# Optimization experiments

Hardware: AMD Instinct MI355X
Metric: run time of the kernel (lower is better)

## Reference

```python
import jax, jax.numpy as jnp
import numpy as np

TIME_SCALE = 10.0
EPS = 1e-5


def _ln(x, g, b):
    m = jnp.mean(x, axis=-1, keepdims=True)
    v = jnp.mean((x - m) ** 2, axis=-1, keepdims=True)
    return (x - m) * jax.lax.rsqrt(v + EPS) * g + b


def setup_inputs() -> dict:
    key = jax.random.key(0)
    ks = jax.random.split(key, 16)
    B, S, D, H, C = 128, 2048, 67, 256, 1

    def lin(k, fan_in, shape):
        return (jax.random.uniform(k, shape, jnp.float32) * 2.0 - 1.0) / np.sqrt(fan_in)

    inp = {
        "x": jax.random.normal(ks[0], (B, S, D), jnp.float32),
        "dt": jax.random.uniform(ks[1], (B, S, 1), jnp.float32),
        # input LayerNorm
        "ln_in_g": jnp.ones((D,), jnp.float32),
        "ln_in_b": jnp.zeros((D,), jnp.float32),
        # feature projection: Linear(D,H) + LayerNorm(H) (+SiLU)
        "proj_W": lin(ks[2], D, (D, H)),
        "proj_b": jnp.zeros((H,), jnp.float32),
        "ln_p_g": jnp.ones((H,), jnp.float32),
        "ln_p_b": jnp.zeros((H,), jnp.float32),
        # CfC cell: four linears from concat([x_t, h]) (2H -> H)
        "W_ff1": lin(ks[3], 2 * H, (2 * H, H)),
        "b_ff1": jnp.zeros((H,), jnp.float32),
        "W_ff2": lin(ks[4], 2 * H, (2 * H, H)),
        "b_ff2": jnp.zeros((H,), jnp.float32),
        "W_ta": lin(ks[5], 2 * H, (2 * H, H)),
        "b_ta": jnp.zeros((H,), jnp.float32),
        "W_tb": lin(ks[6], 2 * H, (2 * H, H)),
        "b_tb": jnp.zeros((H,), jnp.float32),
        # event head: LayerNorm(H) + Linear(H, C)
        "head_g": jnp.ones((H,), jnp.float32),
        "head_b": jnp.zeros((H,), jnp.float32),
        "head_W": lin(ks[7], H, (H, C)),
        "head_bias": jnp.zeros((C,), jnp.float32),
    }
    return inp


def reference(x, dt, ln_in_g, ln_in_b, proj_W, proj_b, ln_p_g, ln_p_b,
              W_ff1, b_ff1, W_ff2, b_ff2, W_ta, b_ta, W_tb, b_tb,
              head_g, head_b, head_W, head_bias):
    B = x.shape[0]
    H = W_ff1.shape[1]

    xn = _ln(x, ln_in_g, ln_in_b)                      # [B,S,D]
    feat = jax.nn.silu(_ln(xn @ proj_W + proj_b, ln_p_g, ln_p_b))  # [B,S,H]

    xs = jnp.swapaxes(feat, 0, 1)                      # [S,B,H] time-major
    dts = jnp.swapaxes(dt * TIME_SCALE, 0, 1)          # [S,B,1]

    def step(h, inp):
        xt, dtt = inp
        z = jnp.concatenate([xt, h], axis=-1)          # [B,2H]
        ff1 = jnp.tanh(z @ W_ff1 + b_ff1)
        ff2 = jnp.tanh(z @ W_ff2 + b_ff2)
        t_interp = jax.nn.sigmoid((z @ W_ta + b_ta) * dtt + (z @ W_tb + b_tb))
        h_new = ff1 * (1.0 - t_interp) + t_interp * ff2
        return h_new, h_new

    h0 = jnp.zeros((B, H), x.dtype)
    _, hs = jax.lax.scan(step, h0, (xs, dts))          # hs: [S,B,H]
    seq = jnp.swapaxes(hs, 0, 1)                       # [B,S,H]
    logits = _ln(seq, head_g, head_b) @ head_W + head_bias  # [B,S,C]
    return logits
```

## Files before the change

kernel.cpp:

```cpp
#include <hip/hip_runtime.h>


typedef __bf16 bf16x8 __attribute__((ext_vector_type(8)));
typedef float f32x4 __attribute__((ext_vector_type(4)));
typedef int i32x4 __attribute__((ext_vector_type(4)));

#define DEVFN static __device__ __forceinline__

DEVFN float bf2f(unsigned short u){ return __uint_as_float(((unsigned)u) << 16); }
DEVFN unsigned short f2bf(float f){
  unsigned x = __float_as_uint(f);
  return (unsigned short)((x + 0x7FFFu + ((x >> 16) & 1u)) >> 16);
}
DEVFN float sigm(float x){ return 1.f / (1.f + __expf(-x)); }
DEVFN float tanh_f(float x){ return 1.f - 2.f / (__expf(2.f * x) + 1.f); }

#define GLD_LDS16(g, l) \
  __builtin_amdgcn_global_load_lds((const __attribute__((address_space(1))) void*)(g), \
                                   (__attribute__((address_space(3))) void*)(l), 16, 0, 0)

static constexpr int BB = 128;
static constexpr int SS = 2048;
static constexpr int DD = 67;

static constexpr size_t OFF_WXT   = 0;
static constexpr size_t OFF_WQ    = 524288;
static constexpr size_t OFF_SW    = 786432;
static constexpr size_t OFF_BIAS4 = 790528;
static constexpr size_t OFF_PWT   = 794624;
static constexpr size_t OFF_GW    = 843776;
static constexpr size_t OFF_SCAL  = 844800;
static constexpr size_t OFF_HST   = 845824;
static constexpr size_t OFF_FEAT  = 878592;

__global__ __launch_bounds__(256) void prep_kernel(
    const float* __restrict__ proj_W,
    const float* __restrict__ W_ff1, const float* __restrict__ b_ff1,
    const float* __restrict__ W_ff2, const float* __restrict__ b_ff2,
    const float* __restrict__ W_ta,  const float* __restrict__ b_ta,
    const float* __restrict__ W_tb,  const float* __restrict__ b_tb,
    const float* __restrict__ head_g, const float* __restrict__ head_b,
    const float* __restrict__ head_W, const float* __restrict__ head_bias,
    unsigned short* __restrict__ WxT, signed char* __restrict__ wq,
    float* __restrict__ sw, float* __restrict__ bias4,
    unsigned short* __restrict__ PWT, float* __restrict__ gW, float* __restrict__ scal)
{
  __shared__ float red[8];
  int bid = blockIdx.x, t = threadIdx.x;
  int wv = t >> 6, ln = t & 63;
  if (bid < 1024) {
    int J = bid, col = J & 255, which = J >> 8;
    const float* Wsrc = which == 0 ? W_ff1 : which == 1 ? W_ff2 : which == 2 ? W_ta : W_tb;
    const float* bsrc = which == 0 ? b_ff1 : which == 1 ? b_ff2 : which == 2 ? b_ta : b_tb;
    float w = Wsrc[t * 256 + col];
    WxT[J * 256 + t] = f2bf(w);
    if (t == 0) bias4[J] = bsrc[col];
  } else if (bid < 2048) {
    int J = bid - 1024, col = J & 255, which = J >> 8;
    const float* Wsrc = which == 0 ? W_ff1 : which == 1 ? W_ff2 : which == 2 ? W_ta : W_tb;
    float w = Wsrc[(256 + t) * 256 + col];
    float a = fabsf(w);
    for (int m = 32; m >= 1; m >>= 1) a = fmaxf(a, __shfl_xor(a, m, 64));
    if (ln == 0) red[wv] = a;
    __syncthreads();
    a = fmaxf(fmaxf(red[0], red[1]), fmaxf(red[2], red[3]));
    float scale = (a > 0.f) ? a * (1.f / 127.f) : 1.f;
    int q = (int)rintf(w / scale);
    q = q > 127 ? 127 : (q < -127 ? -127 : q);
    {
      int g = which, j = col, k = t;
      int wavw = (g << 1) | (j >> 7);
      int lane = ((k & 63) >> 4) * 16 + (j & 15);
      int tt = (j & 127) >> 4;
      int kt = k >> 6;
      size_t dst = (size_t)(wavw * 64 + lane) * 512 + (size_t)(tt * 4 + kt) * 16 + (size_t)(k & 15);
      wq[dst] = (signed char)q;
    }
    if (t == 0) sw[J] = scale;
  } else {
    for (int idx = t; idx < 256 * 96; idx += 256) {
      int j = idx / 96, d = idx % 96;
      float v = (d < DD) ? proj_W[d * 256 + j] : 0.f;
      PWT[idx] = f2bf(v);
    }
    float gw = head_g[t] * head_W[t];
    gW[t] = gw;
    float bw = head_b[t] * head_W[t];
    float s1 = gw, s2 = bw;
    for (int m = 32; m >= 1; m >>= 1) { s1 += __shfl_xor(s1, m, 64); s2 += __shfl_xor(s2, m, 64); }
    if (ln == 0) { red[wv] = s1; red[4 + wv] = s2; }
    __syncthreads();
    if (t == 0) {
      scal[0] = red[0] + red[1] + red[2] + red[3];
      scal[1] = red[4] + red[5] + red[6] + red[7] + head_bias[0];
    }
  }
}

__global__ __launch_bounds__(512) void feat_kernel(
    const float* __restrict__ x, const float* __restrict__ ln_in_g, const float* __restrict__ ln_in_b,
    const float* __restrict__ proj_b, const float* __restrict__ ln_p_g, const float* __restrict__ ln_p_b,
    const unsigned short* __restrict__ PWT, unsigned short* __restrict__ feat,
    int s0, int C, int cshift)
{
  __shared__ __align__(16) unsigned short XA[64 * 104];
  __shared__ __align__(16) unsigned short XB[256 * 96];
  __shared__ float partS[64][4], partQ[64][4], statM[64], statI[64];
  int tid = threadIdx.x, w = tid >> 6, lane = tid & 63;
  int r0 = blockIdx.x * 64;

  {
    float g1v = (lane < 67) ? ln_in_g[lane] : 0.f;
    float b1v = (lane < 67) ? ln_in_b[lane] : 0.f;
    float g2v = (lane < 3) ? ln_in_g[64 + lane] : 0.f;
    float b2v = (lane < 3) ? ln_in_b[64 + lane] : 0.f;
    for (int i = 0; i < 8; ++i) {
      int rl = w * 8 + i;
      int r = r0 + rl;
      int bb = r >> cshift, cs = r & (C - 1);
      const float* xr = x + (size_t)(bb * SS + s0 + cs) * DD;
      float v0 = (lane < 67) ? xr[lane] : 0.f;
      float v1 = (lane < 3) ? xr[64 + lane] : 0.f;
      float s = v0 + v1, q = v0 * v0 + v1 * v1;
      for (int m = 32; m >= 1; m >>= 1) { s += __shfl_xor(s, m, 64); q += __shfl_xor(q, m, 64); }
      float mean = s * (1.f / 67.f);
      float var = q * (1.f / 67.f) - mean * mean;
      float inv = rsqrtf(var + 1e-5f);
      float xn0 = (v0 - mean) * inv * g1v + b1v;
      float xn1 = (v1 - mean) * inv * g2v + b2v;
      XA[rl * 104 + lane] = (lane < 67) ? f2bf(xn0) : (unsigned short)0;
      if (lane < 40) XA[rl * 104 + 64 + lane] = (lane < 3) ? f2bf(xn1) : (unsigned short)0;
    }
  }
  {
    const unsigned int* src = (const unsigned int*)PWT;
    unsigned int* dst = (unsigned int*)XB;
    for (int idx = tid; idx < 256 * 48; idx += 512) dst[idx] = src[idx];
  }
  __syncthreads();

  int wm = w >> 2, wn = w & 3;
  f32x4 acc[2][4];
  #pragma unroll
  for (int mt = 0; mt < 2; ++mt)
    #pragma unroll
    for (int nt = 0; nt < 4; ++nt) acc[mt][nt] = (f32x4){0.f, 0.f, 0.f, 0.f};
  #pragma unroll
  for (int ks = 0; ks < 3; ++ks) {
    int k = ks * 32 + (lane >> 4) * 8;
    bf16x8 a[2], b[4];
    #pragma unroll
    for (int mt = 0; mt < 2; ++mt) {
      int row = wm * 32 + mt * 16 + (lane & 15);
      a[mt] = *reinterpret_cast<const bf16x8*>(&XA[row * 104 + k]);
    }
    #pragma unroll
    for (int nt = 0; nt < 4; ++nt) {
      int col = wn * 64 + nt * 16 + (lane & 15);
      b[nt] = *reinterpret_cast<const bf16x8*>(&XB[col * 96 + k]);
    }
    #pragma unroll
    for (int mt = 0; mt < 2; ++mt)
      #pragma unroll
      for (int nt = 0; nt < 4; ++nt)
        acc[mt][nt] = __builtin_amdgcn_mfma_f32_16x16x32_bf16(a[mt], b[nt], acc[mt][nt], 0, 0, 0);
  }
  #pragma unroll
  for (int nt = 0; nt < 4; ++nt) {
    int col = wn * 64 + nt * 16 + (lane & 15);
    float pb = proj_b[col];
    #pragma unroll
    for (int mt = 0; mt < 2; ++mt)
      #pragma unroll
      for (int r = 0; r < 4; ++r) acc[mt][nt][r] += pb;
  }
  #pragma unroll
  for (int mt = 0; mt < 2; ++mt) {
    #pragma unroll
    for (int r = 0; r < 4; ++r) {
      float s = 0.f, q = 0.f;
      #pragma unroll
      for (int nt = 0; nt < 4; ++nt) { float v = acc[mt][nt][r]; s += v; q += v * v; }
      for (int m = 1; m < 16; m <<= 1) { s += __shfl_xor(s, m, 16); q += __shfl_xor(q, m, 16); }
      if ((lane & 15) == 0) {
        int row = wm * 32 + mt * 16 + (lane >> 4) * 4 + r;
        partS[row][wn] = s; partQ[row][wn] = q;
      }
    }
  }
  __syncthreads();
  if (tid < 64) {
    float s = partS[tid][0] + partS[tid][1] + partS[tid][2] + partS[tid][3];
    float q = partQ[tid][0] + partQ[tid][1] + partQ[tid][2] + partQ[tid][3];
    float mean = s * (1.f / 256.f);
    float var = q * (1.f / 256.f) - mean * mean;
    statM[tid] = mean; statI[tid] = rsqrtf(var + 1e-5f);
  }
  __syncthreads();
  #pragma unroll
  for (int nt = 0; nt < 4; ++nt) {
    int col = wn * 64 + nt * 16 + (lane & 15);
    float gc = ln_p_g[col], bc = ln_p_b[col];
    #pragma unroll
    for (int mt = 0; mt < 2; ++mt)
      #pragma unroll
      for (int r = 0; r < 4; ++r) {
        int row = wm * 32 + mt * 16 + (lane >> 4) * 4 + r;
        float v = acc[mt][nt][r];
        float y = (v - statM[row]) * statI[row] * gc + bc;
        float sl = y * sigm(y);
        feat[(size_t)(r0 + row) * 256 + col] = f2bf(sl);
      }
  }
}

__global__ __launch_bounds__(256, 2) void gemm_kernel(
    const unsigned short* __restrict__ feat, const unsigned short* __restrict__ WxT,
    const float* __restrict__ bias4, unsigned short* __restrict__ pre)
{
  __shared__ __align__(16) unsigned short Abuf[128 * 64];
  __shared__ __align__(16) unsigned short Bbuf[128 * 64];
  int tid = threadIdx.x, w = tid >> 6, lane = tid & 63;
  int m0 = blockIdx.x * 128, n0 = blockIdx.y * 128;
  int wm = w >> 1, wn = w & 1;
  f32x4 acc[4][4];
  #pragma unroll
  for (int i = 0; i < 4; ++i)
    #pragma unroll
    for (int j = 0; j < 4; ++j) acc[i][j] = (f32x4){0.f, 0.f, 0.f, 0.f};

  #pragma unroll 1
  for (int ks = 0; ks < 4; ++ks) {
    int k0 = ks * 64;
    #pragma unroll
    for (int i = 0; i < 4; ++i) {
      int c = i * 256 + tid;
      int row = c >> 3, cc = c & 7;
      const unsigned short* ga = feat + (size_t)(m0 + row) * 256 + (k0 + cc * 8);
      const unsigned short* gb = WxT + (size_t)(n0 + row) * 256 + (k0 + cc * 8);
      char* la = (char*)Abuf + (size_t)(i * 256 + w * 64) * 16;
      char* lb = (char*)Bbuf + (size_t)(i * 256 + w * 64) * 16;
      GLD_LDS16(ga, la);
      GLD_LDS16(gb, lb);
    }
    __syncthreads();
    #pragma unroll
    for (int kk = 0; kk < 2; ++kk) {
      int k = kk * 32 + (lane >> 4) * 8;
      bf16x8 a[4], b[4];
      #pragma unroll
      for (int mt = 0; mt < 4; ++mt) {
        int row = wm * 64 + mt * 16 + (lane & 15);
        a[mt] = *reinterpret_cast<const bf16x8*>(&Abuf[row * 64 + k]);
      }
      #pragma unroll
      for (int nt = 0; nt < 4; ++nt) {
        int col = wn * 64 + nt * 16 + (lane & 15);
        b[nt] = *reinterpret_cast<const bf16x8*>(&Bbuf[col * 64 + k]);
      }
      #pragma unroll
      for (int mt = 0; mt < 4; ++mt)
        #pragma unroll
        for (int nt = 0; nt < 4; ++nt)
          acc[mt][nt] = __builtin_amdgcn_mfma_f32_16x16x32_bf16(a[mt], b[nt], acc[mt][nt], 0, 0, 0);
    }
    __syncthreads();
  }
  #pragma unroll
  for (int nt = 0; nt < 4; ++nt) {
    int col = n0 + wn * 64 + nt * 16 + (lane & 15);
    float bv = bias4[col];
    #pragma unroll
    for (int mt = 0; mt < 4; ++mt)
      #pragma unroll
      for (int r = 0; r < 4; ++r) {
        int row = m0 + wm * 64 + mt * 16 + (lane >> 4) * 4 + r;
        pre[(size_t)row * 1024 + col] = f2bf(acc[mt][nt][r] + bv);
      }
  }
}

#define WRA(n, val) asm volatile("v_accvgpr_write_b32 a" #n ", %0" :: "v"(val) : "a" #n)
#define WR4(n0,n1,n2,n3, q) \
  do { WRA(n0,(q).x); WRA(n1,(q).y); WRA(n2,(q).z); WRA(n3,(q).w); } while (0)
#define MFMA_AB(acc, af, b0, b1) \
  asm volatile("v_mfma_i32_16x16x64_i8 %0, %1, a[" #b0 ":" #b1 "], %2" \
               : "=&v"(acc) : "v"(af), "v"(acc))

__global__ __attribute__((amdgpu_flat_work_group_size(512, 512)))
           __attribute__((amdgpu_waves_per_eu(2, 2)))
void scan_kernel(
    const unsigned short* __restrict__ pre, const float* __restrict__ dt,
    const signed char* __restrict__ wq, const float* __restrict__ sw,
    int* __restrict__ hstate, unsigned short* __restrict__ hseq, int s0, int C)
{
  __shared__ int hq2[2][64];
  __shared__ int gsh[1024];
  int tid = threadIdx.x, w = tid >> 6, l = tid & 63;
  int b = blockIdx.x;

  {
    const int4* wp = (const int4*)(wq + (size_t)tid * 512);
    int4 q0, q1, q2, q3, q4, q5, q6, q7;
    q0=wp[0]; q1=wp[1]; q2=wp[2]; q3=wp[3]; q4=wp[4]; q5=wp[5]; q6=wp[6]; q7=wp[7];
    WR4(0,1,2,3,q0);     WR4(4,5,6,7,q1);     WR4(8,9,10,11,q2);    WR4(12,13,14,15,q3);
    WR4(16,17,18,19,q4); WR4(20,21,22,23,q5); WR4(24,25,26,27,q6);  WR4(28,29,30,31,q7);
    q0=wp[8]; q1=wp[9]; q2=wp[10]; q3=wp[11]; q4=wp[12]; q5=wp[13]; q6=wp[14]; q7=wp[15];
    WR4(32,33,34,35,q0); WR4(36,37,38,39,q1); WR4(40,41,42,43,q2);  WR4(44,45,46,47,q3);
    WR4(48,49,50,51,q4); WR4(52,53,54,55,q5); WR4(56,57,58,59,q6);  WR4(60,61,62,63,q7);
    q0=wp[16]; q1=wp[17]; q2=wp[18]; q3=wp[19]; q4=wp[20]; q5=wp[21]; q6=wp[22]; q7=wp[23];
    WR4(64,65,66,67,q0); WR4(68,69,70,71,q1); WR4(72,73,74,75,q2);  WR4(76,77,78,79,q3);
    WR4(80,81,82,83,q4); WR4(84,85,86,87,q5); WR4(88,89,90,91,q6);  WR4(92,93,94,95,q7);
    q0=wp[24]; q1=wp[25]; q2=wp[26]; q3=wp[27]; q4=wp[28]; q5=wp[29]; q6=wp[30]; q7=wp[31];
    WR4(96,97,98,99,q0);   WR4(100,101,102,103,q1); WR4(104,105,106,107,q2); WR4(108,109,110,111,q3);
    WR4(112,113,114,115,q4); WR4(116,117,118,119,q5); WR4(120,121,122,123,q6); WR4(124,125,126,127,q7);
  }

  float sc0 = 0.f, sc1 = 0.f, sc2 = 0.f, sc3 = 0.f;
  unsigned short pu0 = 0, pu1 = 0, pu2 = 0, pu3 = 0;
  float dtc = 0.f;
  const unsigned short* preB = pre + (size_t)b * C * 1024;
  unsigned short* hsB = hseq + (size_t)b * C * 256;
  if (tid < 256) {
    sc0 = sw[tid]       * (1.f / 127.f);
    sc1 = sw[256 + tid] * (1.f / 127.f);
    sc2 = sw[512 + tid] * (1.f / 127.f);
    sc3 = sw[768 + tid] * (1.f / 127.f);
    pu0 = preB[tid]; pu1 = preB[256 + tid]; pu2 = preB[512 + tid]; pu3 = preB[768 + tid];
    dtc = dt[b * SS + s0] * 10.f;
  }

  if (tid < 64) hq2[0][tid] = (s0 == 0) ? 0 : hstate[b * 64 + tid];
  int cur = 0;
  __syncthreads();

  for (int cs = 0; cs < C; ++cs) {
    const char* hb = (const char*)hq2[cur];
    int aoff = (l >> 4) << 4;
    i32x4 A0 = *reinterpret_cast<const i32x4*>(hb + 0 * 64 + aoff);
    i32x4 A1 = *reinterpret_cast<const i32x4*>(hb + 1 * 64 + aoff);
    i32x4 A2 = *reinterpret_cast<const i32x4*>(hb + 2 * 64 + aoff);
    i32x4 A3 = *reinterpret_cast<const i32x4*>(hb + 3 * 64 + aoff);
    i32x4 c0 = {0,0,0,0}, c1 = {0,0,0,0}, c2 = {0,0,0,0}, c3 = {0,0,0,0};
    i32x4 c4 = {0,0,0,0}, c5 = {0,0,0,0}, c6 = {0,0,0,0}, c7 = {0,0,0,0};
    MFMA_AB(c0, A0,   0,   3); MFMA_AB(c1, A0,  16,  19); MFMA_AB(c2, A0,  32,  35); MFMA_AB(c3, A0,  48,  51);
    MFMA_AB(c4, A0,  64,  67); MFMA_AB(c5, A0,  80,  83); MFMA_AB(c6, A0,  96,  99); MFMA_AB(c7, A0, 112, 115);
    MFMA_AB(c0, A1,   4,   7); MFMA_AB(c1, A1,  20,  23); MFMA_AB(c2, A1,  36,  39); MFMA_AB(c3, A1,  52,  55);
    MFMA_AB(c4, A1,  68,  71); MFMA_AB(c5, A1,  84,  87); MFMA_AB(c6, A1, 100, 103); MFMA_AB(c7, A1, 116, 119);
    MFMA_AB(c0, A2,   8,  11); MFMA_AB(c1, A2,  24,  27); MFMA_AB(c2, A2,  40,  43); MFMA_AB(c3, A2,  56,  59);
    MFMA_AB(c4, A2,  72,  75); MFMA_AB(c5, A2,  88,  91); MFMA_AB(c6, A2, 104, 107); MFMA_AB(c7, A2, 120, 123);
    MFMA_AB(c0, A3,  12,  15); MFMA_AB(c1, A3,  28,  31); MFMA_AB(c2, A3,  44,  47); MFMA_AB(c3, A3,  60,  63);
    MFMA_AB(c4, A3,  76,  79); MFMA_AB(c5, A3,  92,  95); MFMA_AB(c6, A3, 108, 111); MFMA_AB(c7, A3, 124, 127);
    asm volatile("s_nop 7\n\ts_nop 7\n\ts_nop 7");
    if (l < 16) {
      int p = w * 128 + l;
      gsh[p      ] = c0.x; gsh[p +  16] = c1.x; gsh[p +  32] = c2.x; gsh[p +  48] = c3.x;
      gsh[p +  64] = c4.x; gsh[p +  80] = c5.x; gsh[p +  96] = c6.x; gsh[p + 112] = c7.x;
    }
    __syncthreads();
    if (tid < 256) {
      int d0 = gsh[tid], d1 = gsh[256 + tid], d2 = gsh[512 + tid], d3 = gsh[768 + tid];
      float g0 = (float)d0 * sc0 + bf2f(pu0);
      float g1 = (float)d1 * sc1 + bf2f(pu1);
      float g2 = (float)d2 * sc2 + bf2f(pu2);
      float g3 = (float)d3 * sc3 + bf2f(pu3);
      float f1 = tanh_f(g0), f2 = tanh_f(g1);
      float ti = sigm(g2 * dtc + g3);
      float h = f1 + ti * (f2 - f1);
      int q = (int)rintf(h * 127.f);
      q = q > 127 ? 127 : (q < -127 ? -127 : q);
      ((signed char*)hq2[cur ^ 1])[tid] = (signed char)q;
      hsB[(size_t)cs * 256 + tid] = f2bf(h);
      if (cs + 1 < C) {
        const unsigned short* pn = preB + (size_t)(cs + 1) * 1024;
        pu0 = pn[tid]; pu1 = pn[256 + tid]; pu2 = pn[512 + tid]; pu3 = pn[768 + tid];
        dtc = dt[b * SS + s0 + cs + 1] * 10.f;
      }
    }
    cur ^= 1;
    __syncthreads();
  }
  if (tid < 64) hstate[b * 64 + tid] = hq2[cur][tid];
}

__global__ __launch_bounds__(256) void head_kernel(
    const unsigned short* __restrict__ hseq, const float* __restrict__ gW,
    const float* __restrict__ scal, float* __restrict__ out, int s0, int C, int cshift)
{
  int tid = threadIdx.x, wv = tid >> 6, l = tid & 63;
  int row = blockIdx.x * 4 + wv;
  const unsigned short* hr = hseq + (size_t)row * 256 + l * 4;
  ushort4 u = *reinterpret_cast<const ushort4*>(hr);
  float4 gw = *reinterpret_cast<const float4*>(gW + l * 4);
  float v0 = bf2f(u.x), v1 = bf2f(u.y), v2 = bf2f(u.z), v3 = bf2f(u.w);
  float s1 = v0 + v1 + v2 + v3;
  float s2 = v0 * v0 + v1 * v1 + v2 * v2 + v3 * v3;
  float s3 = v0 * gw.x + v1 * gw.y + v2 * gw.z + v3 * gw.w;
  for (int m = 32; m >= 1; m >>= 1) {
    s1 += __shfl_xor(s1, m, 64); s2 += __shfl_xor(s2, m, 64); s3 += __shfl_xor(s3, m, 64);
  }
  if (l == 0) {
    float mean = s1 * (1.f / 256.f);
    float var = s2 * (1.f / 256.f) - mean * mean;
    float inv = rsqrtf(var + 1e-5f);
    int b = row >> cshift, cs = row & (C - 1);
    out[(size_t)b * SS + s0 + cs] = inv * (s3 - mean * scal[0]) + scal[1];
  }
}

extern "C" void kernel_launch(void* const* d_in, const int* in_sizes, int n_in,
                              void* d_out, int out_size, void* d_ws, size_t ws_size,
                              hipStream_t stream)
{
  (void)in_sizes; (void)n_in; (void)out_size;
  const float* x        = (const float*)d_in[0];
  const float* dt       = (const float*)d_in[1];
  const float* ln_in_g  = (const float*)d_in[2];
  const float* ln_in_b  = (const float*)d_in[3];
  const float* proj_W   = (const float*)d_in[4];
  const float* proj_b   = (const float*)d_in[5];
  const float* ln_p_g   = (const float*)d_in[6];
  const float* ln_p_b   = (const float*)d_in[7];
  const float* W_ff1    = (const float*)d_in[8];
  const float* b_ff1    = (const float*)d_in[9];
  const float* W_ff2    = (const float*)d_in[10];
  const float* b_ff2    = (const float*)d_in[11];
  const float* W_ta     = (const float*)d_in[12];
  const float* b_ta     = (const float*)d_in[13];
  const float* W_tb     = (const float*)d_in[14];
  const float* b_tb     = (const float*)d_in[15];
  const float* head_g   = (const float*)d_in[16];
  const float* head_b   = (const float*)d_in[17];
  const float* head_W   = (const float*)d_in[18];
  const float* head_bias= (const float*)d_in[19];

  char* ws = (char*)d_ws;
  unsigned short* WxT = (unsigned short*)(ws + OFF_WXT);
  signed char* wq     = (signed char*)(ws + OFF_WQ);
  float* sw           = (float*)(ws + OFF_SW);
  float* bias4        = (float*)(ws + OFF_BIAS4);
  unsigned short* PWT = (unsigned short*)(ws + OFF_PWT);
  float* gWv          = (float*)(ws + OFF_GW);
  float* scal         = (float*)(ws + OFF_SCAL);
  int* hstate         = (int*)(ws + OFF_HST);

  int C = 16;
  for (int c = 2048; c >= 16; c >>= 1) {
    size_t need = OFF_FEAT + (size_t)c * 65536 + (size_t)c * 262144;
    if (need <= ws_size) { C = c; break; }
  }
  unsigned short* featb = (unsigned short*)(ws + OFF_FEAT);
  unsigned short* preb  = (unsigned short*)(ws + OFF_FEAT + (size_t)C * 65536);
  int cshift = 31 - __builtin_clz((unsigned)C);

  prep_kernel<<<2049, 256, 0, stream>>>(proj_W, W_ff1, b_ff1, W_ff2, b_ff2, W_ta, b_ta, W_tb, b_tb,
                                        head_g, head_b, head_W, head_bias,
                                        WxT, wq, sw, bias4, PWT, gWv, scal);
  int nch = SS / C;
  for (int ch = 0; ch < nch; ++ch) {
    int s0 = ch * C;
    feat_kernel<<<dim3(BB * C / 64), 512, 0, stream>>>(x, ln_in_g, ln_in_b, proj_b, ln_p_g, ln_p_b,
                                                       PWT, featb, s0, C, cshift);
    gemm_kernel<<<dim3(BB * C / 128, 8), 256, 0, stream>>>(featb, WxT, bias4, preb);
    scan_kernel<<<dim3(BB), 512, 0, stream>>>(preb, dt, wq, sw, hstate, featb, s0, C);
    head_kernel<<<dim3(BB * C / 4), 256, 0, stream>>>(featb, gWv, scal, (float*)d_out, s0, C, cshift);
  }
}
```

Measured before the change: 2.723 ms.

## Relayout int8 recurrent weights so each wave owns all four gates

Reorders the quantized recurrent weight layout so that each wave computes all four gate pre-activations (ff1, ff2, ta, tb) for the same 32 hidden columns, instead of each wave covering one gate over 128 columns. The gate epilogue can then read its MFMA accumulators directly in registers. This removes the LDS round-trip through the gate scratch buffer and one __syncthreads per time step of the serial scan. In exchange the epilogue runs on a subset of lanes in all eight waves rather than on the first four waves.

```diff
diff --git a/kernel.cpp b/kernel.cpp
--- a/kernel.cpp
+++ b/kernel.cpp
@@ -69,11 +69,11 @@
     q = q > 127 ? 127 : (q < -127 ? -127 : q);
     {
       int g = which, j = col, k = t;
-      int wavw = (g << 1) | (j >> 7);
+      int wavw = j >> 5;
       int lane = ((k & 63) >> 4) * 16 + (j & 15);
-      int tt = (j & 127) >> 4;
-      int kt = k >> 6;
-      size_t dst = (size_t)(wavw * 64 + lane) * 512 + (size_t)(tt * 4 + kt) * 16 + (size_t)(k & 15);
+      int tt = (j >> 4) & 1;
+      int f = (g * 2 + tt) * 4 + (k >> 6);
+      size_t dst = (size_t)(wavw * 64 + lane) * 512 + (size_t)f * 16 + (size_t)(k & 15);
       wq[dst] = (signed char)q;
     }
     if (t == 0) sw[J] = scale;
@@ -294,8 +294,7 @@
     const signed char* __restrict__ wq, const float* __restrict__ sw,
     int* __restrict__ hstate, unsigned short* __restrict__ hseq, int s0, int C)
 {
-  __shared__ int hq2[2][64];
-  __shared__ int gsh[1024];
+  __shared__ __align__(16) signed char hq2[2][256];
   int tid = threadIdx.x, w = tid >> 6, l = tid & 63;
   int b = blockIdx.x;
 
@@ -316,27 +315,32 @@
     WR4(112,113,114,115,q4); WR4(116,117,118,119,q5); WR4(120,121,122,123,q6); WR4(124,125,126,127,q7);
   }
 
+  int lg = l >> 4;
+  int tt = lg & 1;
+  bool gact = (lg < 2);
+  int j = w * 32 + tt * 16 + (l & 15);
+
   float sc0 = 0.f, sc1 = 0.f, sc2 = 0.f, sc3 = 0.f;
   unsigned short pu0 = 0, pu1 = 0, pu2 = 0, pu3 = 0;
   float dtc = 0.f;
   const unsigned short* preB = pre + (size_t)b * C * 1024;
   unsigned short* hsB = hseq + (size_t)b * C * 256;
-  if (tid < 256) {
-    sc0 = sw[tid]       * (1.f / 127.f);
-    sc1 = sw[256 + tid] * (1.f / 127.f);
-    sc2 = sw[512 + tid] * (1.f / 127.f);
-    sc3 = sw[768 + tid] * (1.f / 127.f);
-    pu0 = preB[tid]; pu1 = preB[256 + tid]; pu2 = preB[512 + tid]; pu3 = preB[768 + tid];
+  if (gact) {
+    sc0 = sw[j]       * (1.f / 127.f);
+    sc1 = sw[256 + j] * (1.f / 127.f);
+    sc2 = sw[512 + j] * (1.f / 127.f);
+    sc3 = sw[768 + j] * (1.f / 127.f);
+    pu0 = preB[j]; pu1 = preB[256 + j]; pu2 = preB[512 + j]; pu3 = preB[768 + j];
     dtc = dt[b * SS + s0] * 10.f;
   }
 
-  if (tid < 64) hq2[0][tid] = (s0 == 0) ? 0 : hstate[b * 64 + tid];
+  if (tid < 64) ((int*)hq2[0])[tid] = (s0 == 0) ? 0 : hstate[b * 64 + tid];
   int cur = 0;
   __syncthreads();
 
   for (int cs = 0; cs < C; ++cs) {
-    const char* hb = (const char*)hq2[cur];
-    int aoff = (l >> 4) << 4;
+    const signed char* hb = hq2[cur];
+    int aoff = lg << 4;
     i32x4 A0 = *reinterpret_cast<const i32x4*>(hb + 0 * 64 + aoff);
     i32x4 A1 = *reinterpret_cast<const i32x4*>(hb + 1 * 64 + aoff);
     i32x4 A2 = *reinterpret_cast<const i32x4*>(hb + 2 * 64 + aoff);
@@ -352,14 +356,11 @@
     MFMA_AB(c0, A3,  12,  15); MFMA_AB(c1, A3,  28,  31); MFMA_AB(c2, A3,  44,  47); MFMA_AB(c3, A3,  60,  63);
     MFMA_AB(c4, A3,  76,  79); MFMA_AB(c5, A3,  92,  95); MFMA_AB(c6, A3, 108, 111); MFMA_AB(c7, A3, 124, 127);
     asm volatile("s_nop 7\n\ts_nop 7\n\ts_nop 7");
-    if (l < 16) {
-      int p = w * 128 + l;
-      gsh[p      ] = c0.x; gsh[p +  16] = c1.x; gsh[p +  32] = c2.x; gsh[p +  48] = c3.x;
-      gsh[p +  64] = c4.x; gsh[p +  80] = c5.x; gsh[p +  96] = c6.x; gsh[p + 112] = c7.x;
-    }
-    __syncthreads();
-    if (tid < 256) {
-      int d0 = gsh[tid], d1 = gsh[256 + tid], d2 = gsh[512 + tid], d3 = gsh[768 + tid];
+    if (gact) {
+      int d0 = tt ? c1.x : c0.x;
+      int d1 = tt ? c3.x : c2.x;
+      int d2 = tt ? c5.x : c4.x;
+      int d3 = tt ? c7.x : c6.x;
       float g0 = (float)d0 * sc0 + bf2f(pu0);
       float g1 = (float)d1 * sc1 + bf2f(pu1);
       float g2 = (float)d2 * sc2 + bf2f(pu2);
@@ -369,18 +370,18 @@
       float h = f1 + ti * (f2 - f1);
       int q = (int)rintf(h * 127.f);
       q = q > 127 ? 127 : (q < -127 ? -127 : q);
-      ((signed char*)hq2[cur ^ 1])[tid] = (signed char)q;
-      hsB[(size_t)cs * 256 + tid] = f2bf(h);
+      hq2[cur ^ 1][j] = (signed char)q;
+      hsB[(size_t)cs * 256 + j] = f2bf(h);
       if (cs + 1 < C) {
         const unsigned short* pn = preB + (size_t)(cs + 1) * 1024;
-        pu0 = pn[tid]; pu1 = pn[256 + tid]; pu2 = pn[512 + tid]; pu3 = pn[768 + tid];
+        pu0 = pn[j]; pu1 = pn[256 + j]; pu2 = pn[512 + j]; pu3 = pn[768 + j];
         dtc = dt[b * SS + s0 + cs + 1] * 10.f;
       }
     }
     cur ^= 1;
     __syncthreads();
   }
-  if (tid < 64) hstate[b * 64 + tid] = hq2[cur][tid];
+  if (tid < 64) hstate[b * 64 + tid] = ((const int*)hq2[cur])[tid];
 }
 
 __global__ __launch_bounds__(256) void head_kernel(
```

New measurement: 2.569 ms. 1.06x faster.
